# Kernel optimization log

Measured on AMD Instinct MI355X. Metric: run time of the kernel, lower is better.

The kernel has to match this reference:

```python
import jax, jax.numpy as jnp
import numpy as np

K = 3
STRIDE = 1
PADDING = 1


def _conv2d(x, w, b, stride, padding):
    out = jax.lax.conv_general_dilated(
        x, w, window_strides=(stride, stride),
        padding=[(padding, padding), (padding, padding)],
        dimension_numbers=('NCHW', 'OIHW', 'NCHW'))
    return out + b[None, :, None, None]


def _grid_sample_bilinear_zeros(x, grid):
    B, C, Hin, Win = x.shape
    gx = (grid[..., 0] + 1.0) * (Win * 0.5) - 0.5  # (B,Hg,Wg) pixel coords
    gy = (grid[..., 1] + 1.0) * (Hin * 0.5) - 0.5
    x0f = jnp.floor(gx)
    y0f = jnp.floor(gy)
    wx1 = gx - x0f  # bilinear weights
    wy1 = gy - y0f
    x0 = x0f.astype(jnp.int32)
    y0 = y0f.astype(jnp.int32)
    xf = x.reshape(B, C, Hin * Win)

    def gather(yi, xi):
        valid = (xi >= 0) & (xi < Win) & (yi >= 0) & (yi < Hin)  # zero padding
        idx = jnp.clip(yi, 0, Hin - 1) * Win + jnp.clip(xi, 0, Win - 1)
        g = jax.vmap(lambda xb, ib: xb[:, ib])(xf, idx)  # (B,C,Hg,Wg)
        return g * valid[:, None, :, :].astype(x.dtype)

    w00 = ((1.0 - wx1) * (1.0 - wy1))[:, None]
    w01 = (wx1 * (1.0 - wy1))[:, None]
    w10 = ((1.0 - wx1) * wy1)[:, None]
    w11 = (wx1 * wy1)[:, None]
    return (gather(y0, x0) * w00 + gather(y0, x0 + 1) * w01 +
            gather(y0 + 1, x0) * w10 + gather(y0 + 1, x0 + 1) * w11)


def setup_inputs() -> dict:
    key = jax.random.key(0)
    k1, k2, k3 = jax.random.split(key, 3)
    B, C, O, H, W = 8, 128, 128, 64, 64
    x = jax.random.normal(k1, (B, C, H, W), dtype=jnp.float32)
    # small offset-predictor weights so sampled locations stay near the grid
    w_off = jax.random.normal(k2, (2 * K * K, C, K, K), dtype=jnp.float32) * 1e-3
    b_off = jnp.zeros((2 * K * K,), dtype=jnp.float32)
    w_main = jax.random.normal(k3, (O, C, K, K), dtype=jnp.float32) * 0.05
    b_main = jnp.zeros((O,), dtype=jnp.float32)
    return {"x": x, "w_off": w_off, "b_off": b_off, "w_main": w_main, "b_main": b_main}


def reference(x, w_off, b_off, w_main, b_main):
    offset = _conv2d(x, w_off, b_off, STRIDE, PADDING)  # (B, 2*K*K, H, W)
    B, _, H, W = offset.shape
    off = jnp.transpose(offset, (0, 2, 3, 1)).reshape(B, H, W, K, K, 2)
    # The torch in-place loops reduce to:
    #   x-comp: cumsum over i of column j=0, broadcast over j
    #   y-comp: cumsum over j of row    i=0, broadcast over i
    ox = jnp.cumsum(off[:, :, :, :, 0, 0], axis=3)  # (B,H,W,K)
    oy = jnp.cumsum(off[:, :, :, 0, :, 1], axis=3)  # (B,H,W,K)
    ox_f = jnp.broadcast_to(ox[..., None], (B, H, W, K, K))
    oy_f = jnp.broadcast_to(oy[:, :, :, None, :], (B, H, W, K, K))
    off_f = jnp.stack([ox_f, oy_f], axis=-1).reshape(B, H, W, K * K, 2)

    y_range = jnp.linspace(-1.0, 1.0, H, dtype=x.dtype)
    x_range = jnp.linspace(-1.0, 1.0, W, dtype=x.dtype)
    yg, xg = jnp.meshgrid(y_range, x_range, indexing='ij')
    base = jnp.stack((xg, yg), axis=-1)  # (H,W,2)
    grid = base[None, :, :, None, :] + off_f  # (B,H,W,K*K,2)
    grid = grid.reshape(B, H, W * K * K, 2)

    xs = _grid_sample_bilinear_zeros(x, grid)  # (B,C,H,W*K*K)
    C = x.shape[1]
    xs = xs.reshape(B, C, H, W, K * K)
    wm = w_main.reshape(w_main.shape[0], C, K * K)
    out = jnp.einsum('bchwk,ock->bohw', xs, wm)
    return out + b_main[None, :, None, None]
```

## Files before the change

kernel.cpp:

```cpp
#include <hip/hip_runtime.h>
#include <hip/hip_bf16.h>
#include <stdint.h>

typedef unsigned short u16;
typedef unsigned int u32;
typedef __attribute__((ext_vector_type(8))) short short8;
typedef __attribute__((ext_vector_type(4))) float float4v;

#define CH 128
#define OO 128
#define KD 1152
#define MPIX 32768
#define IMB 16

__device__ __forceinline__ u16 f2bf(float v) {
    __hip_bfloat16 h = __float2bfloat16(v);
    return *reinterpret_cast<u16*>(&h);
}

__device__ __forceinline__ float bf_lo(u32 u) {
    u32 t = u << 16;
    return __builtin_bit_cast(float, t);
}
__device__ __forceinline__ float bf_hi(u32 u) {
    u32 t = u & 0xffff0000u;
    return __builtin_bit_cast(float, t);
}
__device__ __forceinline__ u32 pack_bf16(float lo, float hi) {
    u32 ul = __builtin_bit_cast(u32, lo);
    u32 uh = __builtin_bit_cast(u32, hi);
    return ((ul + 0x8000u) >> 16) | ((uh + 0x8000u) & 0xffff0000u);
}

__global__ __launch_bounds__(256) void transpose_kernel(const float* __restrict__ x,
                                                        __hip_bfloat16* __restrict__ xt) {
    __shared__ float st[64][65];
    int tid = threadIdx.x;
    int bh = blockIdx.x;
    int b = bh >> 6;
    int h = bh & 63;
    const float* xb = x + ((size_t)b * CH) * 4096 + (size_t)h * 64;
    __hip_bfloat16* xo = xt + ((size_t)bh << 6) * CH;
    for (int cc0 = 0; cc0 < 128; cc0 += 64) {
        #pragma unroll
        for (int step = 0; step < 16; ++step) {
            int cl = (tid >> 6) + step * 4;
            int w = tid & 63;
            st[cl][w] = xb[(size_t)(cc0 + cl) * 4096 + w];
        }
        __syncthreads();
        #pragma unroll
        for (int step = 0; step < 16; ++step) {
            int w = (tid >> 6) + step * 4;
            int cl = tid & 63;
            xo[(size_t)w * CH + cc0 + cl] = __float2bfloat16(st[cl][w]);
        }
        __syncthreads();
    }
}

__global__ __launch_bounds__(256) void offset_conv_kernel(const float* __restrict__ x,
                                                          const float* __restrict__ w_off,
                                                          float* __restrict__ partial) {
    int tid = threadIdx.x;
    int m = blockIdx.x * 256 + tid;
    int chunk = blockIdx.y;
    int b = m >> 12;
    int hw = m & 4095;
    int h = hw >> 6;
    int w = hw & 63;
    float acc[6] = {0.f, 0.f, 0.f, 0.f, 0.f, 0.f};
    int c0 = chunk * 32;
    for (int c = c0; c < c0 + 32; ++c) {
        const float* xc = x + ((size_t)(b * CH + c) << 12);
        float xv[9];
        #pragma unroll
        for (int dy = 0; dy < 3; ++dy) {
            int yy = h + dy - 1;
            bool vy = (unsigned)yy < 64u;
            #pragma unroll
            for (int dx = 0; dx < 3; ++dx) {
                int xx = w + dx - 1;
                bool vv = vy && ((unsigned)xx < 64u);
                xv[dy * 3 + dx] = vv ? xc[yy * 64 + xx] : 0.f;
            }
        }
        const float* wb = w_off + (size_t)c * 9;
        #pragma unroll
        for (int s = 0; s < 6; ++s) {
            int chn = (s < 3) ? s * 6 : (s - 3) * 2 + 1;
            const float* wp = wb + (size_t)chn * (CH * 9);
            float a = acc[s];
            #pragma unroll
            for (int t = 0; t < 9; ++t) a = fmaf(xv[t], wp[t], a);
            acc[s] = a;
        }
    }
    float* po = partial + ((size_t)(chunk << 15) + m) * 6;
    #pragma unroll
    for (int s = 0; s < 6; ++s) po[s] = acc[s];
}

__global__ __launch_bounds__(256) void wreorder_kernel(const float* __restrict__ w_main,
                                                       u16* __restrict__ Wb) {
    int idx = blockIdx.x * 256 + threadIdx.x;
    if (idx >= OO * KD) return;
    int o = idx / KD;
    int r = idx - o * KD;
    int k = r >> 7;
    int c = r & 127;
    Wb[idx] = f2bf(w_main[(size_t)o * KD + c * 9 + k]);
}

__global__ __launch_bounds__(256) void im2col_kernel(const __hip_bfloat16* __restrict__ xt,
                                                     const float* __restrict__ partial,
                                                     const float* __restrict__ b_off,
                                                     u16* __restrict__ Apix) {
    __shared__ float offs[IMB][6];
    __shared__ float2 gxy[IMB][9];
    int tid = threadIdx.x;
    int m0 = blockIdx.x * IMB;
    int b = m0 >> 12;
    int h = (m0 & 4095) >> 6;
    int w0 = m0 & 63;

    if (tid < IMB * 6) {
        int pix = tid / 6, s = tid % 6;
        int m = m0 + pix;
        int chn = (s < 3) ? s * 6 : (s - 3) * 2 + 1;
        float v = b_off[chn];
        #pragma unroll
        for (int q = 0; q < 4; ++q) v += partial[((size_t)(q << 15) + m) * 6 + s];
        offs[pix][s] = v;
    }
    __syncthreads();
    if (tid < IMB * 9) {
        int pix = tid / 9, k = tid % 9;
        int i = k / 3, j = k - i * 3;
        float ox = offs[pix][0];
        if (i >= 1) ox += offs[pix][1];
        if (i >= 2) ox += offs[pix][2];
        float oy = offs[pix][3];
        if (j >= 1) oy += offs[pix][4];
        if (j >= 2) oy += offs[pix][5];
        const float step = 2.0f / 63.0f;
        float bxn = -1.0f + (w0 + pix) * step;
        float byn = -1.0f + h * step;
        gxy[pix][k] = make_float2(fmaf(bxn + ox, 32.0f, 31.5f),
                                  fmaf(byn + oy, 32.0f, 31.5f));
    }
    __syncthreads();

    int pix = tid >> 4;
    int c8 = (tid & 15) * 8;
    const u32* xb = (const u32*)(xt + (((size_t)b << 12) * CH));
    u16* ao = Apix + (size_t)(m0 + pix) * KD + c8;

    for (int k = 0; k < 9; ++k) {
        float2 g = gxy[pix][k];
        float x0f = floorf(g.x), y0f = floorf(g.y);
        float wx = g.x - x0f, wy = g.y - y0f;
        int ix0 = (int)x0f, iy0 = (int)y0f;
        int ix1 = ix0 + 1, iy1 = iy0 + 1;
        float fx0 = ((unsigned)ix0 < 64u) ? 1.f : 0.f;
        float fx1 = ((unsigned)ix1 < 64u) ? 1.f : 0.f;
        float fy0 = ((unsigned)iy0 < 64u) ? 1.f : 0.f;
        float fy1 = ((unsigned)iy1 < 64u) ? 1.f : 0.f;
        float w00 = (1.f - wy) * (1.f - wx) * fy0 * fx0;
        float w01 = (1.f - wy) * wx * fy0 * fx1;
        float w10 = wy * (1.f - wx) * fy1 * fx0;
        float w11 = wy * wx * fy1 * fx1;
        int cx0 = min(max(ix0, 0), 63), cx1 = min(max(ix1, 0), 63);
        int cy0 = min(max(iy0, 0), 63), cy1 = min(max(iy1, 0), 63);
        int base00 = ((cy0 * 64 + cx0) * CH + c8) >> 1;
        int base01 = ((cy0 * 64 + cx1) * CH + c8) >> 1;
        int base10 = ((cy1 * 64 + cx0) * CH + c8) >> 1;
        int base11 = ((cy1 * 64 + cx1) * CH + c8) >> 1;
        uint4 u00 = *(const uint4*)(xb + base00);
        uint4 u01 = *(const uint4*)(xb + base01);
        uint4 u10 = *(const uint4*)(xb + base10);
        uint4 u11 = *(const uint4*)(xb + base11);
        u32 outp[4];
        const u32* p00 = (const u32*)&u00;
        const u32* p01 = (const u32*)&u01;
        const u32* p10 = (const u32*)&u10;
        const u32* p11 = (const u32*)&u11;
        #pragma unroll
        for (int q = 0; q < 4; ++q) {
            float lo = w00 * bf_lo(p00[q]);
            lo = fmaf(w01, bf_lo(p01[q]), lo);
            lo = fmaf(w10, bf_lo(p10[q]), lo);
            lo = fmaf(w11, bf_lo(p11[q]), lo);
            float hi = w00 * bf_hi(p00[q]);
            hi = fmaf(w01, bf_hi(p01[q]), hi);
            hi = fmaf(w10, bf_hi(p10[q]), hi);
            hi = fmaf(w11, bf_hi(p11[q]), hi);
            outp[q] = pack_bf16(lo, hi);
        }
        *(uint4*)(ao + k * CH) = *(const uint4*)outp;
    }
}

__global__ __launch_bounds__(256) void gemm_kernel(const u16* __restrict__ Wb,
                                                   const u16* __restrict__ Apix,
                                                   const float* __restrict__ b_main,
                                                   float* __restrict__ out) {
    __shared__ __align__(16) u16 lA[64 * 32];
    __shared__ __align__(16) u16 lB[128 * 32];
    int tid = threadIdx.x;
    int wave = tid >> 6;
    int lane = tid & 63;
    int wmh = wave & 1;
    int wn = wave >> 1;
    int ob = blockIdx.y * 64;
    int pb = blockIdx.x * 128;
    int mrow = lane & 15;
    int q8 = (lane >> 4) * 8;

    float4v acc[2][4];
    #pragma unroll
    for (int sm = 0; sm < 2; ++sm)
        #pragma unroll
        for (int sn = 0; sn < 4; ++sn)
            acc[sm][sn] = (float4v){0.f, 0.f, 0.f, 0.f};

    const u16* Ap = Wb + (size_t)ob * KD;
    const u16* Bp = Apix + (size_t)pb * KD;

    int arow = tid >> 2;
    int acol = (tid & 3) * 8;
    int brow0 = tid >> 1;
    int bcol0 = (tid & 1) * 16;

    for (int kk = 0; kk < 36; ++kk) {
        int col0 = kk * 32;
        *(uint4*)&lA[(arow * 32) + acol] = *(const uint4*)(Ap + (size_t)arow * KD + col0 + acol);
        #pragma unroll
        for (int q = 0; q < 2; ++q) {
            int idx = q * 256 + tid;
            int row = idx >> 2;
            int cole = (idx & 3) * 8;
            *(uint4*)&lB[row * 32 + cole] = *(const uint4*)(Bp + (size_t)row * KD + col0 + cole);
        }
        __syncthreads();
        short8 af[2], bfv[4];
        #pragma unroll
        for (int s = 0; s < 2; ++s)
            af[s] = *(const short8*)&lA[(wmh * 32 + s * 16 + mrow) * 32 + q8];
        #pragma unroll
        for (int s = 0; s < 4; ++s)
            bfv[s] = *(const short8*)&lB[(wn * 64 + s * 16 + mrow) * 32 + q8];
        #pragma unroll
        for (int sm = 0; sm < 2; ++sm)
            #pragma unroll
            for (int sn = 0; sn < 4; ++sn)
                acc[sm][sn] = __builtin_amdgcn_mfma_f32_16x16x32_bf16(af[sm], bfv[sn],
                                                                     acc[sm][sn], 0, 0, 0);
        __syncthreads();
    }

    #pragma unroll
    for (int sm = 0; sm < 2; ++sm) {
        int o = ob + wmh * 32 + sm * 16 + (lane >> 4) * 4;
        #pragma unroll
        for (int sn = 0; sn < 4; ++sn) {
            int pcol = pb + wn * 64 + sn * 16 + mrow;
            int b = pcol >> 12;
            int rem = pcol & 4095;
            float* op = out + (((size_t)b * OO) << 12) + rem;
            #pragma unroll
            for (int r = 0; r < 4; ++r)
                op[(size_t)(o + r) << 12] = acc[sm][sn][r] + b_main[o + r];
        }
    }
}

extern "C" void kernel_launch(void* const* d_in, const int* in_sizes, int n_in,
                              void* d_out, int out_size, void* d_ws, size_t ws_size,
                              hipStream_t stream) {
    const float* x      = (const float*)d_in[0];
    const float* w_off  = (const float*)d_in[1];
    const float* b_off  = (const float*)d_in[2];
    const float* w_main = (const float*)d_in[3];
    const float* b_main = (const float*)d_in[4];
    float* out = (float*)d_out;

    char* ws = (char*)d_ws;
    __hip_bfloat16* xt = (__hip_bfloat16*)ws;
    float* partial = (float*)(ws + 8388608);
    u16* Wb   = (u16*)(ws + 8388608 + 3145728);
    u16* Apix = (u16*)(ws + 8388608 + 3145728 + 294912);

    transpose_kernel<<<512, 256, 0, stream>>>(x, xt);
    offset_conv_kernel<<<dim3(128, 4), 256, 0, stream>>>(x, w_off, partial);
    wreorder_kernel<<<576, 256, 0, stream>>>(w_main, Wb);
    im2col_kernel<<<MPIX / IMB, 256, 0, stream>>>(xt, partial, b_off, Apix);
    gemm_kernel<<<dim3(256, 2), 256, 0, stream>>>(Wb, Apix, b_main, out);
}
```

Before: 141.9 us.

## Fuse bilinear im2col sampling into the MFMA GEMM and drop the Apix buffer

Replaces the separate im2col kernel, which wrote a bf16 sampled-patch matrix to global memory, and the GEMM that read it back, with one fused kernel. Each block now covers 64 pixels by all 128 output channels. It precomputes bilinear weights and corner offsets in shared memory, then samples the input on the fly into the LDS B-tile each K step, with register prefetch of the next step's loads. This removes roughly 75 MB of intermediate write and read traffic and one launch. In exchange, gather latency and interpolation ALU now sit inside the GEMM loop, and the grid drops to 512 blocks.

```diff
diff --git a/kernel.cpp b/kernel.cpp
--- a/kernel.cpp
+++ b/kernel.cpp
@@ -11,7 +11,6 @@
 #define OO 128
 #define KD 1152
 #define MPIX 32768
-#define IMB 16
 
 __device__ __forceinline__ u16 f2bf(float v) {
     __hip_bfloat16 h = __float2bfloat16(v);
@@ -112,20 +111,25 @@
     Wb[idx] = f2bf(w_main[(size_t)o * KD + c * 9 + k]);
 }
 
-__global__ __launch_bounds__(256) void im2col_kernel(const __hip_bfloat16* __restrict__ xt,
-                                                     const float* __restrict__ partial,
-                                                     const float* __restrict__ b_off,
-                                                     u16* __restrict__ Apix) {
-    __shared__ float offs[IMB][6];
-    __shared__ float2 gxy[IMB][9];
+__global__ __launch_bounds__(256) void fused_gemm_kernel(const __hip_bfloat16* __restrict__ xt,
+                                                         const float* __restrict__ partial,
+                                                         const float* __restrict__ b_off,
+                                                         const u16* __restrict__ Wb,
+                                                         const float* __restrict__ b_main,
+                                                         float* __restrict__ out) {
+    __shared__ float offs[64][6];
+    __shared__ __align__(16) float4v twt[64][9];
+    __shared__ __align__(16) int4 tbs[64][9];
+    __shared__ __align__(16) u16 lA[128 * 32];
+    __shared__ __align__(16) u16 lB[64 * 32];
+
     int tid = threadIdx.x;
-    int m0 = blockIdx.x * IMB;
+    int m0 = blockIdx.x * 64;
     int b = m0 >> 12;
     int h = (m0 & 4095) >> 6;
-    int w0 = m0 & 63;
-
-    if (tid < IMB * 6) {
-        int pix = tid / 6, s = tid % 6;
+
+    for (int idx = tid; idx < 64 * 6; idx += 256) {
+        int pix = idx / 6, s = idx % 6;
         int m = m0 + pix;
         int chn = (s < 3) ? s * 6 : (s - 3) * 2 + 1;
         float v = b_off[chn];
@@ -134,8 +138,9 @@
         offs[pix][s] = v;
     }
     __syncthreads();
-    if (tid < IMB * 9) {
-        int pix = tid / 9, k = tid % 9;
+
+    for (int idx = tid; idx < 64 * 9; idx += 256) {
+        int pix = idx / 9, k = idx % 9;
         int i = k / 3, j = k - i * 3;
         float ox = offs[pix][0];
         if (i >= 1) ox += offs[pix][1];
@@ -144,128 +149,122 @@
         if (j >= 1) oy += offs[pix][4];
         if (j >= 2) oy += offs[pix][5];
         const float step = 2.0f / 63.0f;
-        float bxn = -1.0f + (w0 + pix) * step;
+        float bxn = -1.0f + pix * step;
         float byn = -1.0f + h * step;
-        gxy[pix][k] = make_float2(fmaf(bxn + ox, 32.0f, 31.5f),
-                                  fmaf(byn + oy, 32.0f, 31.5f));
-    }
-    __syncthreads();
-
-    int pix = tid >> 4;
-    int c8 = (tid & 15) * 8;
-    const u32* xb = (const u32*)(xt + (((size_t)b << 12) * CH));
-    u16* ao = Apix + (size_t)(m0 + pix) * KD + c8;
-
-    for (int k = 0; k < 9; ++k) {
-        float2 g = gxy[pix][k];
-        float x0f = floorf(g.x), y0f = floorf(g.y);
-        float wx = g.x - x0f, wy = g.y - y0f;
+        float gx = fmaf(bxn + ox, 32.0f, 31.5f);
+        float gy = fmaf(byn + oy, 32.0f, 31.5f);
+        float x0f = floorf(gx), y0f = floorf(gy);
+        float wx = gx - x0f, wy = gy - y0f;
         int ix0 = (int)x0f, iy0 = (int)y0f;
         int ix1 = ix0 + 1, iy1 = iy0 + 1;
         float fx0 = ((unsigned)ix0 < 64u) ? 1.f : 0.f;
         float fx1 = ((unsigned)ix1 < 64u) ? 1.f : 0.f;
         float fy0 = ((unsigned)iy0 < 64u) ? 1.f : 0.f;
         float fy1 = ((unsigned)iy1 < 64u) ? 1.f : 0.f;
-        float w00 = (1.f - wy) * (1.f - wx) * fy0 * fx0;
-        float w01 = (1.f - wy) * wx * fy0 * fx1;
-        float w10 = wy * (1.f - wx) * fy1 * fx0;
-        float w11 = wy * wx * fy1 * fx1;
+        float4v wv;
+        wv[0] = (1.f - wy) * (1.f - wx) * fy0 * fx0;
+        wv[1] = (1.f - wy) * wx * fy0 * fx1;
+        wv[2] = wy * (1.f - wx) * fy1 * fx0;
+        wv[3] = wy * wx * fy1 * fx1;
         int cx0 = min(max(ix0, 0), 63), cx1 = min(max(ix1, 0), 63);
         int cy0 = min(max(iy0, 0), 63), cy1 = min(max(iy1, 0), 63);
-        int base00 = ((cy0 * 64 + cx0) * CH + c8) >> 1;
-        int base01 = ((cy0 * 64 + cx1) * CH + c8) >> 1;
-        int base10 = ((cy1 * 64 + cx0) * CH + c8) >> 1;
-        int base11 = ((cy1 * 64 + cx1) * CH + c8) >> 1;
-        uint4 u00 = *(const uint4*)(xb + base00);
-        uint4 u01 = *(const uint4*)(xb + base01);
-        uint4 u10 = *(const uint4*)(xb + base10);
-        uint4 u11 = *(const uint4*)(xb + base11);
-        u32 outp[4];
-        const u32* p00 = (const u32*)&u00;
-        const u32* p01 = (const u32*)&u01;
-        const u32* p10 = (const u32*)&u10;
-        const u32* p11 = (const u32*)&u11;
-        #pragma unroll
-        for (int q = 0; q < 4; ++q) {
-            float lo = w00 * bf_lo(p00[q]);
-            lo = fmaf(w01, bf_lo(p01[q]), lo);
-            lo = fmaf(w10, bf_lo(p10[q]), lo);
-            lo = fmaf(w11, bf_lo(p11[q]), lo);
-            float hi = w00 * bf_hi(p00[q]);
-            hi = fmaf(w01, bf_hi(p01[q]), hi);
-            hi = fmaf(w10, bf_hi(p10[q]), hi);
-            hi = fmaf(w11, bf_hi(p11[q]), hi);
-            outp[q] = pack_bf16(lo, hi);
-        }
-        *(uint4*)(ao + k * CH) = *(const uint4*)outp;
-    }
-}
-
-__global__ __launch_bounds__(256) void gemm_kernel(const u16* __restrict__ Wb,
-                                                   const u16* __restrict__ Apix,
-                                                   const float* __restrict__ b_main,
-                                                   float* __restrict__ out) {
-    __shared__ __align__(16) u16 lA[64 * 32];
-    __shared__ __align__(16) u16 lB[128 * 32];
-    int tid = threadIdx.x;
-    int wave = tid >> 6;
-    int lane = tid & 63;
-    int wmh = wave & 1;
-    int wn = wave >> 1;
-    int ob = blockIdx.y * 64;
-    int pb = blockIdx.x * 128;
+        twt[pix][k] = wv;
+        tbs[pix][k] = make_int4((cy0 * 64 + cx0) * 64, (cy0 * 64 + cx1) * 64,
+                                (cy1 * 64 + cx0) * 64, (cy1 * 64 + cx1) * 64);
+    }
+    __syncthreads();
+
+    int wave = tid >> 6, lane = tid & 63;
+    int wo = wave & 1;
+    int wp = wave >> 1;
     int mrow = lane & 15;
     int q8 = (lane >> 4) * 8;
 
-    float4v acc[2][4];
+    int pix = tid >> 2;
+    int cg = (tid & 3) * 8;
+    const u32* xb = (const u32*)(xt + (((size_t)b << 12) * (size_t)CH));
+    const u16* abase = Wb + (size_t)(tid >> 2) * KD + (tid & 3) * 8;
+    int asto = (tid >> 2) * 32 + (tid & 3) * 8;
+    int bsto = pix * 32 + cg;
+
+    float4v acc[4][2];
     #pragma unroll
-    for (int sm = 0; sm < 2; ++sm)
-        #pragma unroll
-        for (int sn = 0; sn < 4; ++sn)
+    for (int sm = 0; sm < 4; ++sm)
+        #pragma unroll
+        for (int sn = 0; sn < 2; ++sn)
             acc[sm][sn] = (float4v){0.f, 0.f, 0.f, 0.f};
 
-    const u16* Ap = Wb + (size_t)ob * KD;
-    const u16* Bp = Apix + (size_t)pb * KD;
-
-    int arow = tid >> 2;
-    int acol = (tid & 3) * 8;
-    int brow0 = tid >> 1;
-    int bcol0 = (tid & 1) * 16;
+    float4v wv;
+    int4 bv;
+    uint4 u00, u01, u10, u11, a0, a1;
+
+    auto issue = [&](int kk) {
+        if ((kk & 3) == 0) {
+            int k = kk >> 2;
+            wv = twt[pix][k];
+            bv = tbs[pix][k];
+        }
+        const u32* xc = xb + ((((kk & 3) << 5) + cg) >> 1);
+        u00 = *(const uint4*)(xc + bv.x);
+        u01 = *(const uint4*)(xc + bv.y);
+        u10 = *(const uint4*)(xc + bv.z);
+        u11 = *(const uint4*)(xc + bv.w);
+        const u16* ap = abase + kk * 32;
+        a0 = *(const uint4*)ap;
+        a1 = *(const uint4*)(ap + (size_t)64 * KD);
+    };
+
+    issue(0);
 
     for (int kk = 0; kk < 36; ++kk) {
-        int col0 = kk * 32;
-        *(uint4*)&lA[(arow * 32) + acol] = *(const uint4*)(Ap + (size_t)arow * KD + col0 + acol);
-        #pragma unroll
-        for (int q = 0; q < 2; ++q) {
-            int idx = q * 256 + tid;
-            int row = idx >> 2;
-            int cole = (idx & 3) * 8;
-            *(uint4*)&lB[row * 32 + cole] = *(const uint4*)(Bp + (size_t)row * KD + col0 + cole);
-        }
-        __syncthreads();
-        short8 af[2], bfv[4];
+        *(uint4*)&lA[asto] = a0;
+        *(uint4*)&lA[asto + 64 * 32] = a1;
+        {
+            const u32* p00 = (const u32*)&u00;
+            const u32* p01 = (const u32*)&u01;
+            const u32* p10 = (const u32*)&u10;
+            const u32* p11 = (const u32*)&u11;
+            u32 outp[4];
+            #pragma unroll
+            for (int q = 0; q < 4; ++q) {
+                float lo = wv[0] * bf_lo(p00[q]);
+                lo = fmaf(wv[1], bf_lo(p01[q]), lo);
+                lo = fmaf(wv[2], bf_lo(p10[q]), lo);
+                lo = fmaf(wv[3], bf_lo(p11[q]), lo);
+                float hi = wv[0] * bf_hi(p00[q]);
+                hi = fmaf(wv[1], bf_hi(p01[q]), hi);
+                hi = fmaf(wv[2], bf_hi(p10[q]), hi);
+                hi = fmaf(wv[3], bf_hi(p11[q]), hi);
+                outp[q] = pack_bf16(lo, hi);
+            }
+            *(uint4*)&lB[bsto] = *(const uint4*)outp;
+        }
+        __syncthreads();
+
+        if (kk < 35) issue(kk + 1);
+
+        short8 af[4], bfv[2];
+        #pragma unroll
+        for (int s = 0; s < 4; ++s)
+            af[s] = *(const short8*)&lA[(wo * 64 + s * 16 + mrow) * 32 + q8];
         #pragma unroll
         for (int s = 0; s < 2; ++s)
-            af[s] = *(const short8*)&lA[(wmh * 32 + s * 16 + mrow) * 32 + q8];
-        #pragma unroll
-        for (int s = 0; s < 4; ++s)
-            bfv[s] = *(const short8*)&lB[(wn * 64 + s * 16 + mrow) * 32 + q8];
-        #pragma unroll
-        for (int sm = 0; sm < 2; ++sm)
-            #pragma unroll
-            for (int sn = 0; sn < 4; ++sn)
+            bfv[s] = *(const short8*)&lB[(wp * 32 + s * 16 + mrow) * 32 + q8];
+        #pragma unroll
+        for (int sm = 0; sm < 4; ++sm)
+            #pragma unroll
+            for (int sn = 0; sn < 2; ++sn)
                 acc[sm][sn] = __builtin_amdgcn_mfma_f32_16x16x32_bf16(af[sm], bfv[sn],
                                                                      acc[sm][sn], 0, 0, 0);
         __syncthreads();
     }
 
     #pragma unroll
-    for (int sm = 0; sm < 2; ++sm) {
-        int o = ob + wmh * 32 + sm * 16 + (lane >> 4) * 4;
-        #pragma unroll
-        for (int sn = 0; sn < 4; ++sn) {
-            int pcol = pb + wn * 64 + sn * 16 + mrow;
-            int b = pcol >> 12;
+    for (int sm = 0; sm < 4; ++sm) {
+        int o = wo * 64 + sm * 16 + (lane >> 4) * 4;
+        #pragma unroll
+        for (int sn = 0; sn < 2; ++sn) {
+            int pcol = m0 + wp * 32 + sn * 16 + mrow;
             int rem = pcol & 4095;
             float* op = out + (((size_t)b * OO) << 12) + rem;
             #pragma unroll
@@ -289,11 +288,9 @@
     __hip_bfloat16* xt = (__hip_bfloat16*)ws;
     float* partial = (float*)(ws + 8388608);
     u16* Wb   = (u16*)(ws + 8388608 + 3145728);
-    u16* Apix = (u16*)(ws + 8388608 + 3145728 + 294912);
 
     transpose_kernel<<<512, 256, 0, stream>>>(x, xt);
     offset_conv_kernel<<<dim3(128, 4), 256, 0, stream>>>(x, w_off, partial);
     wreorder_kernel<<<576, 256, 0, stream>>>(w_main, Wb);
-    im2col_kernel<<<MPIX / IMB, 256, 0, stream>>>(xt, partial, b_off, Apix);
-    gemm_kernel<<<dim3(256, 2), 256, 0, stream>>>(Wb, Apix, b_main, out);
-}
+    fused_gemm_kernel<<<MPIX / 64, 256, 0, stream>>>(xt, partial, b_off, Wb, b_main, out);
+}
```

New measurement: 137.1 us. 1.04x faster.
